# Optimization experiments

Hardware: AMD Instinct MI355X
Metric: run time of the kernel (lower is better)

Reference implementation:

```python
import jax, jax.numpy as jnp
import numpy as np

B, V = 256, 128000


def setup_inputs() -> dict:
    key = jax.random.key(0)
    k1, k2 = jax.random.split(key)
    logits = jax.random.normal(k1, (B, V), dtype=jnp.float32) * 4.0
    # temperatures in [0.3, 1.2] to avoid division by ~0
    temperatures = jax.random.uniform(k2, (B,), dtype=jnp.float32) * 0.9 + 0.3
    return {"logits": logits, "temperatures": temperatures}


def reference(logits, temperatures):
    # temperature-scaled softmax
    x = logits.astype(jnp.float32) / temperatures[:, None]
    probs = jax.nn.softmax(x, axis=-1)  # (B, V)
    # torch.empty_like(probs).exponential_(1).clamp_min_(1e-10)
    noise = jnp.maximum(
        jax.random.exponential(jax.random.key(42), probs.shape, dtype=jnp.float32),
        1e-10,
    )
    # Gumbel-max style sampling: argmax of probs / Exp(1) noise
    return jnp.argmax(probs / noise, axis=-1)  # (B,) int
```

## Files before the change

### kernel.cpp

```cpp
#include <hip/hip_runtime.h>
#include <stdint.h>
#include <math.h>

#define BB 256
#define ROW 128000
#define SPLITM 32
#define CHUNKM (ROW / SPLITM)
#define GRIDM (BB * SPLITM)
#define THREADS 512
#define WAVES (THREADS / 64)

#define SEED_THREADS 256
#define SEED_STRIDE 496

#define TF_K2 0x1BD11BF0u
#define SMALL_BITS 0x00100000u
#define MIN_L 1.4426950408889634e-10f
#define LN2 0.69314718055994530942f
#define GMAX 33.0f
#define MODE_CNT_THR 1434

__device__ __forceinline__ uint32_t rotl32(uint32_t x, int r) {
    return __builtin_amdgcn_alignbit(x, x, 32 - r);
}

#define R1S(r)        { x0 += x1; x1 = rotl32(x1, (r)) ^ x0; }
#define RI1S(r, A, B) { x1 += (B); x0 = x0 + (A) + x1; x1 = rotl32(x1, (r)) ^ x0; }

__device__ __forceinline__ uint32_t threefry1_xor(uint32_t c) {
    uint32_t x1 = c + 42u;
    uint32_t x0 = x1;
    x1 = rotl32(x1, 13) ^ x0;
    R1S(15) R1S(26) R1S(6)
    RI1S(17, 42u, TF_K2 + 1u)
    R1S(29) R1S(16) R1S(24)
    RI1S(13, TF_K2, 2u)
    R1S(15) R1S(26) R1S(6)
    RI1S(17, 0u, 45u)
    R1S(29) R1S(16) R1S(24)
    RI1S(13, 42u, TF_K2 + 4u)
    R1S(15) R1S(26) R1S(6)
    return (x0 + TF_K2) ^ (x1 + 5u);
}

__device__ __forceinline__ void threefry8_xor(uint32_t c, uint32_t bits[8]) {
    uint32_t x0[8], x1[8];
#pragma unroll
    for (int j = 0; j < 8; ++j) x1[j] = c + (uint32_t)(j + 42);
#pragma unroll
    for (int j = 0; j < 8; ++j) { x0[j] = x1[j]; x1[j] = rotl32(x1[j], 13) ^ x0[j]; }

#define RND(r)                                        \
    do { _Pragma("unroll")                            \
        for (int j = 0; j < 8; ++j) {                 \
            x0[j] += x1[j];                           \
            x1[j] = rotl32(x1[j], (r)) ^ x0[j];       \
        } } while (0)
#define RNDI(r, A, B)                                 \
    do { _Pragma("unroll")                            \
        for (int j = 0; j < 8; ++j) {                 \
            x1[j] += (B);                             \
            x0[j] = x0[j] + (A) + x1[j];              \
            x1[j] = rotl32(x1[j], (r)) ^ x0[j];       \
        } } while (0)

    RND(15); RND(26); RND(6);
    RNDI(17, 42u, TF_K2 + 1u);
    RND(29); RND(16); RND(24);
    RNDI(13, TF_K2, 2u);
    RND(15); RND(26); RND(6);
    RNDI(17, 0u, 45u);
    RND(29); RND(16); RND(24);
    RNDI(13, 42u, TF_K2 + 4u);
    RND(15); RND(26); RND(6);
#undef RND
#undef RNDI

#pragma unroll
    for (int j = 0; j < 8; ++j) bits[j] = (x0[j] + TF_K2) ^ (x1[j] + 5u);
}

__device__ __forceinline__ float noise_negL(uint32_t bits) {
    const float uf = __uint_as_float(0x3F800000u | (bits >> 9));
    const float L = __builtin_amdgcn_logf(2.0f - uf);
    const float u = uf - 1.0f;
    const float es2 = u * fmaf(u, fmaf(u, fmaf(u,
        -0.3606737602222408f, -0.4808983469629878f),
        -0.7213475204444817f), -1.4426950408889634f);
    const float es2c = fminf(es2, -MIN_L);
    return (bits < SMALL_BITS) ? es2c : L;
}

__device__ __forceinline__ float score1(float x, float invT2, uint32_t bits) {
    const float L = noise_negL(bits);
    return fmaf(x, invT2, -__builtin_amdgcn_logf(-L));
}

__device__ __forceinline__ uint32_t f2o(float f) {
    uint32_t u = __float_as_uint(f);
    return (u & 0x80000000u) ? ~u : (u | 0x80000000u);
}

__global__ __launch_bounds__(SEED_THREADS) void premode_kernel(
    const float* __restrict__ logits, const float* __restrict__ temps,
    float* __restrict__ gs0, int* __restrict__ mode) {
    const int b = blockIdx.x;
    const int t = threadIdx.x;
    const float T = temps[b];
    const float invT2 = 1.0f / (T * LN2);
    const int off = t * SEED_STRIDE;
    const float* rowp = logits + (size_t)b * ROW + off;
    const uint32_t cb = (uint32_t)b * ROW + (uint32_t)off;

    const float4 xa = *reinterpret_cast<const float4*>(rowp);
    const float4 xb = *reinterpret_cast<const float4*>(rowp + 4);
    const float xs[8] = {xa.x, xa.y, xa.z, xa.w, xb.x, xb.y, xb.z, xb.w};
    uint32_t bits[8];
    threefry8_xor(cb, bits);

    float bs = -INFINITY;
#pragma unroll
    for (int j = 0; j < 8; ++j) bs = fmaxf(bs, score1(xs[j], invT2, bits[j]));

#pragma unroll
    for (int o = 32; o >= 1; o >>= 1) bs = fmaxf(bs, __shfl_xor(bs, o));
    __shared__ float sred[SEED_THREADS / 64];
    __shared__ int scr[SEED_THREADS / 64];
    const int lane = t & 63, wid = t >> 6;
    if (lane == 0) sred[wid] = bs;
    __syncthreads();
    const float gsv = fmaxf(fmaxf(sred[0], sred[1]), fmaxf(sred[2], sred[3]));

    const float xthr = (gsv - GMAX) * (T * LN2);
    int c = 0;
#pragma unroll
    for (int j = 0; j < 8; ++j) c += (xs[j] > xthr) ? 1 : 0;
#pragma unroll
    for (int o = 32; o >= 1; o >>= 1) c += __shfl_xor(c, o);
    if (lane == 0) scr[wid] = c;
    __syncthreads();
    if (t == 0) {
        const int tot = scr[0] + scr[1] + scr[2] + scr[3];
        gs0[b] = gsv;
        mode[b] = (tot > MODE_CNT_THR) ? 1 : 0;
    }
}

__global__ __launch_bounds__(THREADS) void chunkmax_kernel(
    const float* __restrict__ logits, const int* __restrict__ mode,
    float* __restrict__ cmx, uint32_t* __restrict__ cmi) {
    const int g = blockIdx.x;
    const int b = g >> 5, q = g & 31;
    if (mode[b]) return;
    const float* rowp = logits + (size_t)b * ROW + (size_t)q * CHUNKM;
    const int tid = threadIdx.x;
    const int rel = tid * 8;

    float mx = -INFINITY;
    uint32_t mi = 0u;
    if (rel < CHUNKM) {
        const float4 xa = *reinterpret_cast<const float4*>(rowp + rel);
        const float4 xb = *reinterpret_cast<const float4*>(rowp + rel + 4);
        const float xs[8] = {xa.x, xa.y, xa.z, xa.w, xb.x, xb.y, xb.z, xb.w};
#pragma unroll
        for (int j = 0; j < 8; ++j)
            if (xs[j] > mx) { mx = xs[j]; mi = (uint32_t)(rel + j); }
    }
#pragma unroll
    for (int off = 32; off >= 1; off >>= 1) {
        const float ox = __shfl_xor(mx, off);
        const uint32_t oi = __shfl_xor(mi, off);
        if (ox > mx) { mx = ox; mi = oi; }
    }
    __shared__ float smx[WAVES];
    __shared__ uint32_t smi[WAVES];
    const int lane = tid & 63, wid = tid >> 6;
    if (lane == 0) { smx[wid] = mx; smi[wid] = mi; }
    __syncthreads();
    if (tid == 0) {
        mx = smx[0]; mi = smi[0];
#pragma unroll
        for (int w = 1; w < WAVES; ++w)
            if (smx[w] > mx) { mx = smx[w]; mi = smi[w]; }
        cmx[g] = mx;
        cmi[g] = (uint32_t)(q * CHUNKM) + mi;
    }
}

__global__ __launch_bounds__(THREADS, 4) void sampler_kernel(
    const float* __restrict__ logits, const float* __restrict__ temps,
    const float* __restrict__ gs0, const int* __restrict__ mode,
    const float* __restrict__ cmx, const uint32_t* __restrict__ cmi,
    unsigned long long* __restrict__ parts) {
    __shared__ int scnt;
    __shared__ float s_xthr;
    __shared__ unsigned short qidx[CHUNKM];
    __shared__ unsigned long long sbest[WAVES];

    const int g = blockIdx.x;
    const int b = g >> 5, q = g & 31;
    const int md = mode[b];
    const float T = temps[b];
    const float invT2 = 1.0f / (T * LN2);
    const float* rowp = logits + (size_t)b * ROW + (size_t)q * CHUNKM;
    const uint32_t cbase = (uint32_t)b * ROW + (uint32_t)(q * CHUNKM);
    const int tid = threadIdx.x;
    const int lane = tid & 63;
    const unsigned long long lmask_lt = (1ull << lane) - 1ull;

    if (!md) {
        if (tid == 0) scnt = 0;
        if (tid < SPLITM) {
            const uint32_t idx = cmi[b * SPLITM + tid];
            const float xm = cmx[b * SPLITM + tid];
            float cs = score1(xm, invT2,
                              threefry1_xor((uint32_t)b * ROW + idx));
            cs = fmaxf(cs, gs0[b]);
#pragma unroll
            for (int o = 16; o >= 1; o >>= 1)
                cs = fmaxf(cs, __shfl_xor(cs, o));
            if (tid == 0) s_xthr = (cs - GMAX) * (T * LN2);
        }
        __syncthreads();
    }

    const int rel = tid * 8;
    const bool act = rel < CHUNKM;
    float xs[8];
    if (act) {
        const float4 xa = *reinterpret_cast<const float4*>(rowp + rel);
        const float4 xb = *reinterpret_cast<const float4*>(rowp + rel + 4);
        xs[0]=xa.x; xs[1]=xa.y; xs[2]=xa.z; xs[3]=xa.w;
        xs[4]=xb.x; xs[5]=xb.y; xs[6]=xb.z; xs[7]=xb.w;
    }

    float best_s = -INFINITY;
    uint32_t best_rel = 0u;

    if (md) {
        if (act) {
            uint32_t bits[8];
            threefry8_xor(cbase + (uint32_t)rel, bits);
            float L8[8];
#pragma unroll
            for (int j = 0; j < 8; ++j) {
                const float uf = __uint_as_float(0x3F800000u | (bits[j] >> 9));
                L8[j] = __builtin_amdgcn_logf(2.0f - uf);
            }
            const uint32_t b01 = min(min(bits[0], bits[1]), bits[2]);
            const uint32_t b34 = min(min(bits[3], bits[4]), bits[5]);
            const uint32_t b67 = min(bits[6], bits[7]);
            if (__any(min(min(b01, b34), b67) < SMALL_BITS)) {
#pragma unroll
                for (int j = 0; j < 8; ++j) {
                    const float u = __uint_as_float(0x3F800000u |
                                    (bits[j] >> 9)) - 1.0f;
                    const float es2 = u * fmaf(u, fmaf(u, fmaf(u,
                        -0.3606737602222408f, -0.4808983469629878f),
                        -0.7213475204444817f), -1.4426950408889634f);
                    const float es2c = fminf(es2, -MIN_L);
                    L8[j] = (bits[j] < SMALL_BITS) ? es2c : L8[j];
                }
            }
#pragma unroll
            for (int j = 0; j < 8; ++j) {
                const float s = fmaf(xs[j], invT2,
                                     -__builtin_amdgcn_logf(-L8[j]));
                if (s > best_s) { best_s = s; best_rel = (uint32_t)(rel + j); }
            }
        }
    } else {
        const float xthr = s_xthr;
        if (act) {
#pragma unroll
            for (int j = 0; j < 8; ++j) {
                const bool pass = xs[j] > xthr;
                const unsigned long long mk = __ballot(pass);
                if (mk != 0ull) {
                    int base = 0;
                    if (lane == 0) base = atomicAdd(&scnt, __popcll(mk));
                    base = __builtin_amdgcn_readfirstlane(base);
                    if (pass) {
                        const int pos = base + (int)__popcll(mk & lmask_lt);
                        qidx[pos] = (unsigned short)(rel + j);
                    }
                }
            }
        }
        __syncthreads();
        const int total = scnt;
        for (int i = tid; i < total; i += THREADS) {
            const int r2 = (int)qidx[i];
            const float x = rowp[r2];
            const float s = score1(x, invT2, threefry1_xor(cbase + (uint32_t)r2));
            if (s > best_s) { best_s = s; best_rel = (uint32_t)r2; }
        }
    }

    const uint32_t best_v = (uint32_t)(q * CHUNKM) + best_rel;
    unsigned long long best =
        ((unsigned long long)f2o(best_s) << 32) | (uint32_t)(~best_v);
#pragma unroll
    for (int off = 32; off >= 1; off >>= 1) {
        const unsigned long long o = __shfl_xor(best, off);
        best = (o > best) ? o : best;
    }
    const int wid = tid >> 6;
    if (lane == 0) sbest[wid] = best;
    __syncthreads();
    if (tid == 0) {
        unsigned long long r = sbest[0];
#pragma unroll
        for (int w = 1; w < WAVES; ++w) r = (sbest[w] > r) ? sbest[w] : r;
        parts[g] = r;
    }
}

__global__ __launch_bounds__(BB) void combine_kernel(
    const unsigned long long* __restrict__ parts, int* __restrict__ out) {
    const int b = threadIdx.x;
    const unsigned long long* p = parts + b * SPLITM;
    unsigned long long r = p[0];
#pragma unroll
    for (int w = 1; w < SPLITM; ++w) r = (p[w] > r) ? p[w] : r;
    out[b] = (int)(~(uint32_t)(r & 0xFFFFFFFFull));
}

extern "C" void kernel_launch(void* const* d_in, const int* in_sizes, int n_in,
                              void* d_out, int out_size, void* d_ws, size_t ws_size,
                              hipStream_t stream) {
    const float* logits = (const float*)d_in[0];
    const float* temps = (const float*)d_in[1];
    int* out = (int*)d_out;
    float* cmx = (float*)d_ws;
    uint32_t* cmi = (uint32_t*)((char*)d_ws + 32768);
    float* gs0 = (float*)((char*)d_ws + 65536);
    int* mode = (int*)((char*)d_ws + 66560);
    unsigned long long* parts =
        (unsigned long long*)((char*)d_ws + 67584);

    hipLaunchKernelGGL(premode_kernel, dim3(BB), dim3(SEED_THREADS), 0, stream,
                       logits, temps, gs0, mode);
    hipLaunchKernelGGL(chunkmax_kernel, dim3(GRIDM), dim3(THREADS), 0, stream,
                       logits, mode, cmx, cmi);
    hipLaunchKernelGGL(sampler_kernel, dim3(GRIDM), dim3(THREADS), 0, stream,
                       logits, temps, gs0, mode, cmx, cmi, parts);
    hipLaunchKernelGGL(combine_kernel, dim3(1), dim3(BB), 0, stream, parts, out);
}
```

Baseline: 77.45 us.

## Queue threshold candidates during chunk scan and skip dense RNG in mode-1 rows

The chunk-max pass now also compacts, per chunk, the logits above a conservative threshold derived from the premode seed score into a global (value, index) queue. The sampler then reads only the queued candidates instead of re-reading the whole chunk, and falls back to a full rescan when the queue overflows. In the dense mode, each thread now computes an upper bound from its max logit and the smallest random bits, and skips the log and score evaluation when no lane can beat the seed score. This trades an extra global write of candidates and more workspace for fewer logit re-reads and fewer transcendental evaluations, with the risk that the bound is wrong or the fallback path costs more.

```diff
diff --git a/kernel.cpp b/kernel.cpp
--- a/kernel.cpp
+++ b/kernel.cpp
@@ -12,6 +12,8 @@
 
 #define SEED_THREADS 256
 #define SEED_STRIDE 496
+
+#define CAP_Q 2048
 
 #define TF_K2 0x1BD11BF0u
 #define SMALL_BITS 0x00100000u
@@ -146,16 +148,28 @@
     }
 }
 
-__global__ __launch_bounds__(THREADS) void chunkmax_kernel(
-    const float* __restrict__ logits, const int* __restrict__ mode,
-    float* __restrict__ cmx, uint32_t* __restrict__ cmi) {
+__global__ __launch_bounds__(THREADS) void chunkscan_kernel(
+    const float* __restrict__ logits, const float* __restrict__ temps,
+    const float* __restrict__ gs0, const int* __restrict__ mode,
+    float* __restrict__ cmx, uint32_t* __restrict__ cmi,
+    int* __restrict__ qcnt, uint2* __restrict__ queue) {
     const int g = blockIdx.x;
     const int b = g >> 5, q = g & 31;
     if (mode[b]) return;
+    __shared__ int scnt;
+    __shared__ float smx[WAVES];
+    __shared__ uint32_t smi[WAVES];
+    const int tid = threadIdx.x;
+    const int lane = tid & 63;
+    const unsigned long long lmask_lt = (1ull << lane) - 1ull;
+    if (tid == 0) scnt = 0;
+    __syncthreads();
+
+    const float xthr = (gs0[b] - GMAX) * (temps[b] * LN2);
     const float* rowp = logits + (size_t)b * ROW + (size_t)q * CHUNKM;
-    const int tid = threadIdx.x;
+    uint2* qp = queue + (size_t)g * CAP_Q;
+
     const int rel = tid * 8;
-
     float mx = -INFINITY;
     uint32_t mi = 0u;
     if (rel < CHUNKM) {
@@ -165,6 +179,22 @@
 #pragma unroll
         for (int j = 0; j < 8; ++j)
             if (xs[j] > mx) { mx = xs[j]; mi = (uint32_t)(rel + j); }
+#pragma unroll
+        for (int j = 0; j < 8; ++j) {
+            const bool pass = xs[j] > xthr;
+            const unsigned long long mk = __ballot(pass);
+            if (mk != 0ull) {
+                int base = 0;
+                if (lane == 0) base = atomicAdd(&scnt, __popcll(mk));
+                base = __builtin_amdgcn_readfirstlane(base);
+                if (pass) {
+                    const int pos = base + (int)__popcll(mk & lmask_lt);
+                    if (pos < CAP_Q)
+                        qp[pos] = make_uint2(__float_as_uint(xs[j]),
+                                             (uint32_t)(rel + j));
+                }
+            }
+        }
     }
 #pragma unroll
     for (int off = 32; off >= 1; off >>= 1) {
@@ -172,9 +202,7 @@
         const uint32_t oi = __shfl_xor(mi, off);
         if (ox > mx) { mx = ox; mi = oi; }
     }
-    __shared__ float smx[WAVES];
-    __shared__ uint32_t smi[WAVES];
-    const int lane = tid & 63, wid = tid >> 6;
+    const int wid = tid >> 6;
     if (lane == 0) { smx[wid] = mx; smi[wid] = mi; }
     __syncthreads();
     if (tid == 0) {
@@ -184,6 +212,7 @@
             if (smx[w] > mx) { mx = smx[w]; mi = smi[w]; }
         cmx[g] = mx;
         cmi[g] = (uint32_t)(q * CHUNKM) + mi;
+        qcnt[g] = scnt;
     }
 }
 
@@ -191,6 +220,7 @@
     const float* __restrict__ logits, const float* __restrict__ temps,
     const float* __restrict__ gs0, const int* __restrict__ mode,
     const float* __restrict__ cmx, const uint32_t* __restrict__ cmi,
+    const int* __restrict__ qcnt, const uint2* __restrict__ queue,
     unsigned long long* __restrict__ parts) {
     __shared__ int scnt;
     __shared__ float s_xthr;
@@ -202,98 +232,123 @@
     const int md = mode[b];
     const float T = temps[b];
     const float invT2 = 1.0f / (T * LN2);
+    const float gs0v = gs0[b];
     const float* rowp = logits + (size_t)b * ROW + (size_t)q * CHUNKM;
     const uint32_t cbase = (uint32_t)b * ROW + (uint32_t)(q * CHUNKM);
     const int tid = threadIdx.x;
     const int lane = tid & 63;
     const unsigned long long lmask_lt = (1ull << lane) - 1ull;
 
-    if (!md) {
+    float best_s = -INFINITY;
+    uint32_t best_rel = 0u;
+    const int rel = tid * 8;
+    const bool act = rel < CHUNKM;
+
+    if (md) {
+        if (act) {
+            const float4 xa = *reinterpret_cast<const float4*>(rowp + rel);
+            const float4 xb = *reinterpret_cast<const float4*>(rowp + rel + 4);
+            const float xs[8] = {xa.x, xa.y, xa.z, xa.w,
+                                 xb.x, xb.y, xb.z, xb.w};
+            uint32_t bits[8];
+            threefry8_xor(cbase + (uint32_t)rel, bits);
+
+            const float x01 = fmaxf(fmaxf(xs[0], xs[1]), fmaxf(xs[2], xs[3]));
+            const float x45 = fmaxf(fmaxf(xs[4], xs[5]), fmaxf(xs[6], xs[7]));
+            const float xmax = fmaxf(x01, x45);
+            const float thrf = 512.0f + __builtin_amdgcn_exp2f(
+                fmaf(xmax, invT2, 31.571f - gs0v));
+            const uint32_t b01 = min(min(bits[0], bits[1]), bits[2]);
+            const uint32_t b34 = min(min(bits[3], bits[4]), bits[5]);
+            const uint32_t b67 = min(bits[6], bits[7]);
+            const uint32_t bmin = min(min(b01, b34), b67);
+
+            if (__any((float)bmin < thrf)) {
+                float L8[8];
+#pragma unroll
+                for (int j = 0; j < 8; ++j) {
+                    const float uf = __uint_as_float(0x3F800000u |
+                                                     (bits[j] >> 9));
+                    L8[j] = __builtin_amdgcn_logf(2.0f - uf);
+                }
+                if (__any(bmin < SMALL_BITS)) {
+#pragma unroll
+                    for (int j = 0; j < 8; ++j) {
+                        const float u = __uint_as_float(0x3F800000u |
+                                        (bits[j] >> 9)) - 1.0f;
+                        const float es2 = u * fmaf(u, fmaf(u, fmaf(u,
+                            -0.3606737602222408f, -0.4808983469629878f),
+                            -0.7213475204444817f), -1.4426950408889634f);
+                        const float es2c = fminf(es2, -MIN_L);
+                        L8[j] = (bits[j] < SMALL_BITS) ? es2c : L8[j];
+                    }
+                }
+#pragma unroll
+                for (int j = 0; j < 8; ++j) {
+                    const float s = fmaf(xs[j], invT2,
+                                         -__builtin_amdgcn_logf(-L8[j]));
+                    if (s > best_s) { best_s = s; best_rel = (uint32_t)(rel + j); }
+                }
+            }
+        }
+    } else {
         if (tid == 0) scnt = 0;
         if (tid < SPLITM) {
             const uint32_t idx = cmi[b * SPLITM + tid];
             const float xm = cmx[b * SPLITM + tid];
             float cs = score1(xm, invT2,
                               threefry1_xor((uint32_t)b * ROW + idx));
-            cs = fmaxf(cs, gs0[b]);
+            cs = fmaxf(cs, gs0v);
 #pragma unroll
             for (int o = 16; o >= 1; o >>= 1)
                 cs = fmaxf(cs, __shfl_xor(cs, o));
             if (tid == 0) s_xthr = (cs - GMAX) * (T * LN2);
         }
         __syncthreads();
-    }
-
-    const int rel = tid * 8;
-    const bool act = rel < CHUNKM;
-    float xs[8];
-    if (act) {
-        const float4 xa = *reinterpret_cast<const float4*>(rowp + rel);
-        const float4 xb = *reinterpret_cast<const float4*>(rowp + rel + 4);
-        xs[0]=xa.x; xs[1]=xa.y; xs[2]=xa.z; xs[3]=xa.w;
-        xs[4]=xb.x; xs[5]=xb.y; xs[6]=xb.z; xs[7]=xb.w;
-    }
-
-    float best_s = -INFINITY;
-    uint32_t best_rel = 0u;
-
-    if (md) {
-        if (act) {
-            uint32_t bits[8];
-            threefry8_xor(cbase + (uint32_t)rel, bits);
-            float L8[8];
-#pragma unroll
-            for (int j = 0; j < 8; ++j) {
-                const float uf = __uint_as_float(0x3F800000u | (bits[j] >> 9));
-                L8[j] = __builtin_amdgcn_logf(2.0f - uf);
+        const float xthr = s_xthr;
+        const int nq = qcnt[g];
+
+        if (nq <= CAP_Q) {
+            const uint2* qp = queue + (size_t)g * CAP_Q;
+            for (int i = tid; i < nq; i += THREADS) {
+                const uint2 e = qp[i];
+                const float x = __uint_as_float(e.x);
+                if (x > xthr) {
+                    const float s = score1(x, invT2,
+                                           threefry1_xor(cbase + e.y));
+                    if (s > best_s) { best_s = s; best_rel = e.y; }
+                }
             }
-            const uint32_t b01 = min(min(bits[0], bits[1]), bits[2]);
-            const uint32_t b34 = min(min(bits[3], bits[4]), bits[5]);
-            const uint32_t b67 = min(bits[6], bits[7]);
-            if (__any(min(min(b01, b34), b67) < SMALL_BITS)) {
+        } else {
+            if (act) {
+                const float4 xa = *reinterpret_cast<const float4*>(rowp + rel);
+                const float4 xb = *reinterpret_cast<const float4*>(rowp + rel + 4);
+                const float xs[8] = {xa.x, xa.y, xa.z, xa.w,
+                                     xb.x, xb.y, xb.z, xb.w};
 #pragma unroll
                 for (int j = 0; j < 8; ++j) {
-                    const float u = __uint_as_float(0x3F800000u |
-                                    (bits[j] >> 9)) - 1.0f;
-                    const float es2 = u * fmaf(u, fmaf(u, fmaf(u,
-                        -0.3606737602222408f, -0.4808983469629878f),
-                        -0.7213475204444817f), -1.4426950408889634f);
-                    const float es2c = fminf(es2, -MIN_L);
-                    L8[j] = (bits[j] < SMALL_BITS) ? es2c : L8[j];
+                    const bool pass = xs[j] > xthr;
+                    const unsigned long long mk = __ballot(pass);
+                    if (mk != 0ull) {
+                        int base = 0;
+                        if (lane == 0) base = atomicAdd(&scnt, __popcll(mk));
+                        base = __builtin_amdgcn_readfirstlane(base);
+                        if (pass) {
+                            const int pos = base + (int)__popcll(mk & lmask_lt);
+                            qidx[pos] = (unsigned short)(rel + j);
+                        }
+                    }
                 }
             }
-#pragma unroll
-            for (int j = 0; j < 8; ++j) {
-                const float s = fmaf(xs[j], invT2,
-                                     -__builtin_amdgcn_logf(-L8[j]));
-                if (s > best_s) { best_s = s; best_rel = (uint32_t)(rel + j); }
+            __syncthreads();
+            const int total = scnt;
+            for (int i = tid; i < total; i += THREADS) {
+                const int r2 = (int)qidx[i];
+                const float x = rowp[r2];
+                const float s = score1(x, invT2,
+                                       threefry1_xor(cbase + (uint32_t)r2));
+                if (s > best_s) { best_s = s; best_rel = (uint32_t)r2; }
             }
-        }
-    } else {
-        const float xthr = s_xthr;
-        if (act) {
-#pragma unroll
-            for (int j = 0; j < 8; ++j) {
-                const bool pass = xs[j] > xthr;
-                const unsigned long long mk = __ballot(pass);
-                if (mk != 0ull) {
-                    int base = 0;
-                    if (lane == 0) base = atomicAdd(&scnt, __popcll(mk));
-                    base = __builtin_amdgcn_readfirstlane(base);
-                    if (pass) {
-                        const int pos = base + (int)__popcll(mk & lmask_lt);
-                        qidx[pos] = (unsigned short)(rel + j);
-                    }
-                }
-            }
-        }
-        __syncthreads();
-        const int total = scnt;
-        for (int i = tid; i < total; i += THREADS) {
-            const int r2 = (int)qidx[i];
-            const float x = rowp[r2];
-            const float s = score1(x, invT2, threefry1_xor(cbase + (uint32_t)r2));
-            if (s > best_s) { best_s = s; best_rel = (uint32_t)r2; }
         }
     }
 
@@ -338,12 +393,14 @@
     int* mode = (int*)((char*)d_ws + 66560);
     unsigned long long* parts =
         (unsigned long long*)((char*)d_ws + 67584);
+    int* qcnt = (int*)((char*)d_ws + 133120);
+    uint2* queue = (uint2*)((char*)d_ws + 165888);
 
     hipLaunchKernelGGL(premode_kernel, dim3(BB), dim3(SEED_THREADS), 0, stream,
                        logits, temps, gs0, mode);
-    hipLaunchKernelGGL(chunkmax_kernel, dim3(GRIDM), dim3(THREADS), 0, stream,
-                       logits, mode, cmx, cmi);
+    hipLaunchKernelGGL(chunkscan_kernel, dim3(GRIDM), dim3(THREADS), 0, stream,
+                       logits, temps, gs0, mode, cmx, cmi, qcnt, queue);
     hipLaunchKernelGGL(sampler_kernel, dim3(GRIDM), dim3(THREADS), 0, stream,
-                       logits, temps, gs0, mode, cmx, cmi, parts);
+                       logits, temps, gs0, mode, cmx, cmi, qcnt, queue, parts);
     hipLaunchKernelGGL(combine_kernel, dim3(1), dim3(BB), 0, stream, parts, out);
 }
```

Measured after the change: 85.30 us. 1.1x slower.

## Run full-eval rows in the chunk-max pass and prune only the remaining rows

Applied to the files above, without the earlier changes.

The chunk-max kernel and the sampler kernel are reorganized. Rows in mode 1 (full Gumbel evaluation) are now handled inside the first pass, and rows in mode 0 only compute chunk maxima there. The second kernel then exits early for mode-1 rows and does the threshold pruning and drain only for mode-0 rows. This removes one redundant read of mode-1 rows and balances work across the two passes. The cost is that the first kernel now carries heavier code for some blocks, which may raise register pressure.

```diff
diff --git a/kernel.cpp b/kernel.cpp
--- a/kernel.cpp
+++ b/kernel.cpp
@@ -146,86 +146,24 @@
     }
 }
 
-__global__ __launch_bounds__(THREADS) void chunkmax_kernel(
-    const float* __restrict__ logits, const int* __restrict__ mode,
-    float* __restrict__ cmx, uint32_t* __restrict__ cmi) {
-    const int g = blockIdx.x;
-    const int b = g >> 5, q = g & 31;
-    if (mode[b]) return;
-    const float* rowp = logits + (size_t)b * ROW + (size_t)q * CHUNKM;
-    const int tid = threadIdx.x;
-    const int rel = tid * 8;
-
-    float mx = -INFINITY;
-    uint32_t mi = 0u;
-    if (rel < CHUNKM) {
-        const float4 xa = *reinterpret_cast<const float4*>(rowp + rel);
-        const float4 xb = *reinterpret_cast<const float4*>(rowp + rel + 4);
-        const float xs[8] = {xa.x, xa.y, xa.z, xa.w, xb.x, xb.y, xb.z, xb.w};
-#pragma unroll
-        for (int j = 0; j < 8; ++j)
-            if (xs[j] > mx) { mx = xs[j]; mi = (uint32_t)(rel + j); }
-    }
-#pragma unroll
-    for (int off = 32; off >= 1; off >>= 1) {
-        const float ox = __shfl_xor(mx, off);
-        const uint32_t oi = __shfl_xor(mi, off);
-        if (ox > mx) { mx = ox; mi = oi; }
-    }
+__global__ __launch_bounds__(THREADS, 4) void eval_or_max_kernel(
+    const float* __restrict__ logits, const float* __restrict__ temps,
+    const float* __restrict__ gs0, const int* __restrict__ mode,
+    float* __restrict__ cmx, uint32_t* __restrict__ cmi,
+    unsigned long long* __restrict__ parts) {
     __shared__ float smx[WAVES];
     __shared__ uint32_t smi[WAVES];
-    const int lane = tid & 63, wid = tid >> 6;
-    if (lane == 0) { smx[wid] = mx; smi[wid] = mi; }
-    __syncthreads();
-    if (tid == 0) {
-        mx = smx[0]; mi = smi[0];
-#pragma unroll
-        for (int w = 1; w < WAVES; ++w)
-            if (smx[w] > mx) { mx = smx[w]; mi = smi[w]; }
-        cmx[g] = mx;
-        cmi[g] = (uint32_t)(q * CHUNKM) + mi;
-    }
-}
-
-__global__ __launch_bounds__(THREADS, 4) void sampler_kernel(
-    const float* __restrict__ logits, const float* __restrict__ temps,
-    const float* __restrict__ gs0, const int* __restrict__ mode,
-    const float* __restrict__ cmx, const uint32_t* __restrict__ cmi,
-    unsigned long long* __restrict__ parts) {
-    __shared__ int scnt;
-    __shared__ float s_xthr;
-    __shared__ unsigned short qidx[CHUNKM];
     __shared__ unsigned long long sbest[WAVES];
 
     const int g = blockIdx.x;
     const int b = g >> 5, q = g & 31;
     const int md = mode[b];
-    const float T = temps[b];
-    const float invT2 = 1.0f / (T * LN2);
     const float* rowp = logits + (size_t)b * ROW + (size_t)q * CHUNKM;
-    const uint32_t cbase = (uint32_t)b * ROW + (uint32_t)(q * CHUNKM);
     const int tid = threadIdx.x;
-    const int lane = tid & 63;
-    const unsigned long long lmask_lt = (1ull << lane) - 1ull;
-
-    if (!md) {
-        if (tid == 0) scnt = 0;
-        if (tid < SPLITM) {
-            const uint32_t idx = cmi[b * SPLITM + tid];
-            const float xm = cmx[b * SPLITM + tid];
-            float cs = score1(xm, invT2,
-                              threefry1_xor((uint32_t)b * ROW + idx));
-            cs = fmaxf(cs, gs0[b]);
-#pragma unroll
-            for (int o = 16; o >= 1; o >>= 1)
-                cs = fmaxf(cs, __shfl_xor(cs, o));
-            if (tid == 0) s_xthr = (cs - GMAX) * (T * LN2);
-        }
-        __syncthreads();
-    }
-
+    const int lane = tid & 63, wid = tid >> 6;
     const int rel = tid * 8;
     const bool act = rel < CHUNKM;
+
     float xs[8];
     if (act) {
         const float4 xa = *reinterpret_cast<const float4*>(rowp + rel);
@@ -234,10 +172,11 @@
         xs[4]=xb.x; xs[5]=xb.y; xs[6]=xb.z; xs[7]=xb.w;
     }
 
-    float best_s = -INFINITY;
-    uint32_t best_rel = 0u;
-
     if (md) {
+        const float invT2 = 1.0f / (temps[b] * LN2);
+        const uint32_t cbase = (uint32_t)b * ROW + (uint32_t)(q * CHUNKM);
+        float best_s = -INFINITY;
+        uint32_t best_rel = 0u;
         if (act) {
             uint32_t bits[8];
             threefry8_xor(cbase + (uint32_t)rel, bits);
@@ -269,32 +208,117 @@
                 if (s > best_s) { best_s = s; best_rel = (uint32_t)(rel + j); }
             }
         }
+        const uint32_t best_v = (uint32_t)(q * CHUNKM) + best_rel;
+        unsigned long long best =
+            ((unsigned long long)f2o(best_s) << 32) | (uint32_t)(~best_v);
+#pragma unroll
+        for (int off = 32; off >= 1; off >>= 1) {
+            const unsigned long long o = __shfl_xor(best, off);
+            best = (o > best) ? o : best;
+        }
+        if (lane == 0) sbest[wid] = best;
+        __syncthreads();
+        if (tid == 0) {
+            unsigned long long r = sbest[0];
+#pragma unroll
+            for (int w = 1; w < WAVES; ++w) r = (sbest[w] > r) ? sbest[w] : r;
+            parts[g] = r;
+        }
     } else {
-        const float xthr = s_xthr;
+        float mx = -INFINITY;
+        uint32_t mi = 0u;
         if (act) {
 #pragma unroll
-            for (int j = 0; j < 8; ++j) {
-                const bool pass = xs[j] > xthr;
-                const unsigned long long mk = __ballot(pass);
-                if (mk != 0ull) {
-                    int base = 0;
-                    if (lane == 0) base = atomicAdd(&scnt, __popcll(mk));
-                    base = __builtin_amdgcn_readfirstlane(base);
-                    if (pass) {
-                        const int pos = base + (int)__popcll(mk & lmask_lt);
-                        qidx[pos] = (unsigned short)(rel + j);
-                    }
+            for (int j = 0; j < 8; ++j)
+                if (xs[j] > mx) { mx = xs[j]; mi = (uint32_t)(rel + j); }
+        }
+#pragma unroll
+        for (int off = 32; off >= 1; off >>= 1) {
+            const float ox = __shfl_xor(mx, off);
+            const uint32_t oi = __shfl_xor(mi, off);
+            if (ox > mx) { mx = ox; mi = oi; }
+        }
+        if (lane == 0) { smx[wid] = mx; smi[wid] = mi; }
+        __syncthreads();
+        if (tid == 0) {
+            mx = smx[0]; mi = smi[0];
+#pragma unroll
+            for (int w = 1; w < WAVES; ++w)
+                if (smx[w] > mx) { mx = smx[w]; mi = smi[w]; }
+            cmx[g] = mx;
+            cmi[g] = (uint32_t)(q * CHUNKM) + mi;
+        }
+    }
+}
+
+__global__ __launch_bounds__(THREADS, 4) void prune_drain_kernel(
+    const float* __restrict__ logits, const float* __restrict__ temps,
+    const float* __restrict__ gs0, const int* __restrict__ mode,
+    const float* __restrict__ cmx, const uint32_t* __restrict__ cmi,
+    unsigned long long* __restrict__ parts) {
+    const int g = blockIdx.x;
+    const int b = g >> 5, q = g & 31;
+    if (mode[b]) return;
+
+    __shared__ int scnt;
+    __shared__ float s_xthr;
+    __shared__ unsigned short qidx[CHUNKM];
+    __shared__ unsigned long long sbest[WAVES];
+
+    const float T = temps[b];
+    const float invT2 = 1.0f / (T * LN2);
+    const float* rowp = logits + (size_t)b * ROW + (size_t)q * CHUNKM;
+    const uint32_t cbase = (uint32_t)b * ROW + (uint32_t)(q * CHUNKM);
+    const int tid = threadIdx.x;
+    const int lane = tid & 63;
+    const unsigned long long lmask_lt = (1ull << lane) - 1ull;
+
+    if (tid == 0) scnt = 0;
+    if (tid < SPLITM) {
+        const uint32_t idx = cmi[b * SPLITM + tid];
+        const float xm = cmx[b * SPLITM + tid];
+        float cs = score1(xm, invT2,
+                          threefry1_xor((uint32_t)b * ROW + idx));
+        cs = fmaxf(cs, gs0[b]);
+#pragma unroll
+        for (int o = 16; o >= 1; o >>= 1)
+            cs = fmaxf(cs, __shfl_xor(cs, o));
+        if (tid == 0) s_xthr = (cs - GMAX) * (T * LN2);
+    }
+    __syncthreads();
+    const float xthr = s_xthr;
+
+    const int rel = tid * 8;
+    const bool act = rel < CHUNKM;
+    float best_s = -INFINITY;
+    uint32_t best_rel = 0u;
+
+    if (act) {
+        const float4 xa = *reinterpret_cast<const float4*>(rowp + rel);
+        const float4 xb = *reinterpret_cast<const float4*>(rowp + rel + 4);
+        const float xs[8] = {xa.x, xa.y, xa.z, xa.w, xb.x, xb.y, xb.z, xb.w};
+#pragma unroll
+        for (int j = 0; j < 8; ++j) {
+            const bool pass = xs[j] > xthr;
+            const unsigned long long mk = __ballot(pass);
+            if (mk != 0ull) {
+                int base = 0;
+                if (lane == 0) base = atomicAdd(&scnt, __popcll(mk));
+                base = __builtin_amdgcn_readfirstlane(base);
+                if (pass) {
+                    const int pos = base + (int)__popcll(mk & lmask_lt);
+                    qidx[pos] = (unsigned short)(rel + j);
                 }
             }
         }
-        __syncthreads();
-        const int total = scnt;
-        for (int i = tid; i < total; i += THREADS) {
-            const int r2 = (int)qidx[i];
-            const float x = rowp[r2];
-            const float s = score1(x, invT2, threefry1_xor(cbase + (uint32_t)r2));
-            if (s > best_s) { best_s = s; best_rel = (uint32_t)r2; }
-        }
+    }
+    __syncthreads();
+    const int total = scnt;
+    for (int i = tid; i < total; i += THREADS) {
+        const int r2 = (int)qidx[i];
+        const float x = rowp[r2];
+        const float s = score1(x, invT2, threefry1_xor(cbase + (uint32_t)r2));
+        if (s > best_s) { best_s = s; best_rel = (uint32_t)r2; }
     }
 
     const uint32_t best_v = (uint32_t)(q * CHUNKM) + best_rel;
@@ -341,9 +365,9 @@
 
     hipLaunchKernelGGL(premode_kernel, dim3(BB), dim3(SEED_THREADS), 0, stream,
                        logits, temps, gs0, mode);
-    hipLaunchKernelGGL(chunkmax_kernel, dim3(GRIDM), dim3(THREADS), 0, stream,
-                       logits, mode, cmx, cmi);
-    hipLaunchKernelGGL(sampler_kernel, dim3(GRIDM), dim3(THREADS), 0, stream,
+    hipLaunchKernelGGL(eval_or_max_kernel, dim3(GRIDM), dim3(THREADS), 0, stream,
+                       logits, temps, gs0, mode, cmx, cmi, parts);
+    hipLaunchKernelGGL(prune_drain_kernel, dim3(GRIDM), dim3(THREADS), 0, stream,
                        logits, temps, gs0, mode, cmx, cmi, parts);
     hipLaunchKernelGGL(combine_kernel, dim3(1), dim3(BB), 0, stream, parts, out);
 }
```

Result: slower. 79.13 us (+2.2%).
